# Kernel optimization log

Measured on AMD Instinct MI355X. Metric: run time of the kernel, lower is better.

The kernel has to match this reference:

```python
import jax, jax.numpy as jnp
import numpy as np

B, S, D = 2, 2048, 4096
H, KV, HD = 32, 8, 128          # n_heads, n_kv_heads, head_dim
N_REP = H // KV                  # GQA repeat factor = 4
ROPE_THETA = 500000.0


def _rope_tables(seqlen, head_dim, theta):
    inv_freq = 1.0 / (theta ** (np.arange(0, head_dim, 2, dtype=np.float32) / head_dim))
    angles = np.outer(np.arange(seqlen, dtype=np.float32), inv_freq)  # [S, HD/2]
    return jnp.asarray(np.cos(angles)), jnp.asarray(np.sin(angles))


def setup_inputs() -> dict:
    key = jax.random.key(0)
    ks = jax.random.split(key, 6)
    x = jax.random.normal(ks[0], (B, S, D), dtype=jnp.float32)
    freqs_cos, freqs_sin = _rope_tables(S, HD, ROPE_THETA)
    # causal additive mask, broadcast over (batch, heads)
    mask = jnp.where(jnp.tril(jnp.ones((S, S), dtype=bool)), 0.0, -jnp.inf).astype(jnp.float32)
    sc = 0.02
    wq = sc * jax.random.normal(ks[1], (D, H * HD), dtype=jnp.float32)   # (in, out)
    wk = sc * jax.random.normal(ks[2], (D, KV * HD), dtype=jnp.float32)
    wv = sc * jax.random.normal(ks[3], (D, KV * HD), dtype=jnp.float32)
    wo = sc * jax.random.normal(ks[4], (H * HD, D), dtype=jnp.float32)
    return {"x": x, "freqs_cos": freqs_cos, "freqs_sin": freqs_sin, "mask": mask,
            "wq": wq, "wk": wk, "wv": wv, "wo": wo}


def _apply_rope(t, cos, sin):
    # t: [B, S, nh, HD]; cos/sin: [S, HD/2]. Complex rotation on adjacent pairs.
    t2 = t.reshape(*t.shape[:-1], HD // 2, 2)
    t0, t1 = t2[..., 0], t2[..., 1]
    c = cos[None, :, None, :]
    s = sin[None, :, None, :]
    r0 = t0 * c - t1 * s
    r1 = t0 * s + t1 * c
    return jnp.stack([r0, r1], axis=-1).reshape(t.shape)


def reference(x, freqs_cos, freqs_sin, mask, wq, wk, wv, wo):
    bsz, seqlen, _ = x.shape
    xq = (x @ wq).reshape(bsz, seqlen, H, HD)
    xk = (x @ wk).reshape(bsz, seqlen, KV, HD)
    xv = (x @ wv).reshape(bsz, seqlen, KV, HD)
    xq = _apply_rope(xq, freqs_cos, freqs_sin)
    xk = _apply_rope(xk, freqs_cos, freqs_sin)
    # repeat_kv (GQA) -> [B, S, H, HD]
    keys = jnp.repeat(xk, N_REP, axis=2)
    values = jnp.repeat(xv, N_REP, axis=2)
    scores = jnp.einsum('bqhd,bkhd->bhqk', xq, keys) / jnp.sqrt(jnp.float32(HD))
    scores = scores + mask[None, None, :, :]
    probs = jax.nn.softmax(scores.astype(jnp.float32), axis=-1).astype(xq.dtype)
    out = jnp.einsum('bhqk,bkhd->bqhd', probs, values).reshape(bsz, seqlen, H * HD)
    return out @ wo
```

## Files before the change

### kernel.cpp

```cpp
#include <hip/hip_runtime.h>
#include <stdint.h>

#define B_ 2
#define S_ 2048
#define D_ 4096
#define H_ 32
#define KV_ 8
#define HD_ 128
#define M_ (B_*S_)
#define NQ_ (H_*HD_)
#define NKV_ (KV_*HD_)

typedef unsigned short u16;
typedef __bf16 bf16x8 __attribute__((ext_vector_type(8)));
typedef float f32x4 __attribute__((ext_vector_type(4)));
typedef u16 u16x8 __attribute__((ext_vector_type(8)));
typedef u16 u16x4 __attribute__((ext_vector_type(4)));

__device__ __forceinline__ u16 f2bf(float f) {
  union { float f; unsigned u; } v; v.f = f;
  unsigned r = v.u + 0x7fffu + ((v.u >> 16) & 1u);
  return (u16)(r >> 16);
}
__device__ __forceinline__ u16 f2bft(float f) {
  union { float f; unsigned u; } v; v.f = f;
  return (u16)(v.u >> 16);
}
__device__ __forceinline__ float bf2f(u16 u) {
  union { unsigned u; float f; } v; v.u = ((unsigned)u) << 16;
  return v.f;
}
__device__ __forceinline__ f32x4 mfma16(bf16x8 a, bf16x8 b, f32x4 c) {
  return __builtin_amdgcn_mfma_f32_16x16x32_bf16(a, b, c, 0, 0, 0);
}

#define GLDS16(gp, lp) __builtin_amdgcn_global_load_lds( \
    (const __attribute__((address_space(1))) unsigned int*)(gp), \
    (__attribute__((address_space(3))) unsigned int*)(lp), 16, 0, 0)

__global__ __launch_bounds__(256) void cvt_bf16(const float* __restrict__ in,
                                                u16* __restrict__ out, int n) {
  int i = (blockIdx.x * 256 + threadIdx.x) * 8;
  if (i >= n) return;
  float4 a = *(const float4*)(in + i);
  float4 b = *(const float4*)(in + i + 4);
  u16x8 o;
  o[0]=f2bf(a.x); o[1]=f2bf(a.y); o[2]=f2bf(a.z); o[3]=f2bf(a.w);
  o[4]=f2bf(b.x); o[5]=f2bf(b.y); o[6]=f2bf(b.z); o[7]=f2bf(b.w);
  *(u16x8*)(out + i) = o;
}

__global__ __launch_bounds__(256) void tcvt(const float* __restrict__ in,
                                            u16* __restrict__ out, int R, int C) {
  __shared__ float tf[64][65];
  int c0 = blockIdx.x * 64, r0 = blockIdx.y * 64;
  int l16 = threadIdx.x & 15, r16 = threadIdx.x >> 4;
  #pragma unroll
  for (int p = 0; p < 4; ++p) {
    int r = p * 16 + r16;
    float4 v = *(const float4*)(in + (size_t)(r0 + r) * C + c0 + l16 * 4);
    tf[r][l16 * 4 + 0] = v.x; tf[r][l16 * 4 + 1] = v.y;
    tf[r][l16 * 4 + 2] = v.z; tf[r][l16 * 4 + 3] = v.w;
  }
  __syncthreads();
  int oc = threadIdx.x >> 2, ch = threadIdx.x & 3;
  u16x8 o1, o2;
  #pragma unroll
  for (int i = 0; i < 8; ++i) o1[i] = f2bf(tf[ch * 16 + i][oc]);
  #pragma unroll
  for (int i = 0; i < 8; ++i) o2[i] = f2bf(tf[ch * 16 + 8 + i][oc]);
  *(u16x8*)(out + (size_t)(c0 + oc) * R + r0 + ch * 16) = o1;
  *(u16x8*)(out + (size_t)(c0 + oc) * R + r0 + ch * 16 + 8) = o2;
}

template<int OUTMODE, bool DOROPE>
__global__ __launch_bounds__(512, 2) void gemm256(const u16* __restrict__ A,
    const u16* __restrict__ BT, void* __restrict__ Cv,
    const float* __restrict__ FC, const float* __restrict__ FS,
    int M, int N, int K) {
  extern __shared__ __attribute__((aligned(16))) u16 DL[];
  const int tid = threadIdx.x;
  const int nbx = N >> 8;
  const int cpx = gridDim.x >> 3;
  const int swzb = (blockIdx.x & 7) * cpx + (blockIdx.x >> 3);
  const int bn0 = (swzb % nbx) << 8, bm0 = (swzb / nbx) << 8;
  const int l = tid & 63, g = l >> 4, q = l & 15;
  const int w = tid >> 6;
  const int wm = (w >> 2) * 128, wn = (w & 3) * 64;
  const int nt = K >> 5;
  f32x4 acc[8][4] = {};

  const int srow = tid >> 2, schunk = tid & 3;
  const int ssw = (schunk ^ ((srow >> 1) & 3)) << 3;
  const u16* gA0 = A  + (size_t)(bm0 + srow) * K + ssw;
  const u16* gA1 = gA0 + (size_t)128 * K;
  const u16* gB0 = BT + (size_t)(bn0 + srow) * K + ssw;
  const u16* gB1 = gB0 + (size_t)128 * K;

  auto STAGE = [&](int t) {
    const int kt = t << 5;
    u16* d = DL + (t % 3) * 16384;
    GLDS16(gA0 + kt, d + tid * 8);
    GLDS16(gA1 + kt, d + 4096 + tid * 8);
    GLDS16(gB0 + kt, d + 8192 + tid * 8);
    GLDS16(gB1 + kt, d + 12288 + tid * 8);
  };

  const u16* ra = DL + (wm + q) * 32 + ((g ^ (((wm + q) >> 1) & 3)) << 3);
  const u16* rb = DL + 8192 + (wn + q) * 32 + ((g ^ (((wn + q) >> 1) & 3)) << 3);

  bf16x8 aC[8], aN[8], bC[4], bN[4];

  STAGE(0); STAGE(1);
  asm volatile("s_waitcnt vmcnt(4)" ::: "memory");
  __builtin_amdgcn_s_barrier();
  #pragma unroll
  for (int m = 0; m < 8; ++m) aC[m] = *(const bf16x8*)(ra + m * 512);
  #pragma unroll
  for (int n = 0; n < 4; ++n) bC[n] = *(const bf16x8*)(rb + n * 512);

  auto TILE = [&](int t, bf16x8 (&ac)[8], bf16x8 (&bc)[4],
                         bf16x8 (&an)[8], bf16x8 (&bn)[4]) {
    if (t + 2 < nt) {
      STAGE(t + 2);
      asm volatile("s_waitcnt vmcnt(4)" ::: "memory");
    } else {
      asm volatile("s_waitcnt vmcnt(0)" ::: "memory");
    }
    __builtin_amdgcn_s_barrier();
    if (t + 1 < nt) {
      const u16* pa = ra + ((t + 1) % 3) * 16384;
      const u16* pb = rb + ((t + 1) % 3) * 16384;
      #pragma unroll
      for (int m = 0; m < 8; ++m) an[m] = *(const bf16x8*)(pa + m * 512);
      #pragma unroll
      for (int n = 0; n < 4; ++n) bn[n] = *(const bf16x8*)(pb + n * 512);
    }
    __builtin_amdgcn_s_setprio(1);
    #pragma unroll
    for (int m = 0; m < 8; ++m) {
      acc[m][0] = mfma16(ac[m], bc[0], acc[m][0]);
      acc[m][1] = mfma16(ac[m], bc[1], acc[m][1]);
      acc[m][2] = mfma16(ac[m], bc[2], acc[m][2]);
      acc[m][3] = mfma16(ac[m], bc[3], acc[m][3]);
    }
    __builtin_amdgcn_s_setprio(0);
  };

  for (int t = 0; t < nt; t += 2) {
    TILE(t,     aC, bC, aN, bN);
    TILE(t + 1, aN, bN, aC, bC);
  }

  #pragma unroll
  for (int m = 0; m < 8; ++m)
    #pragma unroll
    for (int n = 0; n < 4; ++n) {
      const int col = bn0 + wn + n * 16 + q;
      if (DOROPE) {
        const int fi = (col & 127) >> 1;
        const float sgn = (q & 1) ? 1.0f : -1.0f;
        #pragma unroll
        for (int j = 0; j < 4; ++j) {
          int row = bm0 + wm + m * 16 + g * 4 + j;
          int pos = row & (S_ - 1);
          float c = FC[pos * 64 + fi], s = FS[pos * 64 + fi];
          float own = acc[m][n][j];
          float par = __shfl_xor(own, 1);
          ((u16*)Cv)[(size_t)row * N + col] = f2bf(own * c + par * s * sgn);
        }
      } else {
        #pragma unroll
        for (int j = 0; j < 4; ++j) {
          size_t off = (size_t)(bm0 + wm + m * 16 + g * 4 + j) * N + col;
          if (OUTMODE == 1) ((float*)Cv)[off] = acc[m][n][j];
          else              ((u16*)Cv)[off]  = f2bf(acc[m][n][j]);
        }
      }
    }
}

__global__ __launch_bounds__(512, 2) void gemm_kv(const u16* __restrict__ A,
    const u16* __restrict__ BT, u16* __restrict__ Ck, u16* __restrict__ Cvt,
    const float* __restrict__ FC, const float* __restrict__ FS,
    int M, int N, int K) {
  extern __shared__ __attribute__((aligned(16))) u16 DL[];
  const int tid = threadIdx.x;
  const int nbx = N >> 7;
  const int cpx = gridDim.x >> 3;
  const int swzb = (blockIdx.x & 7) * cpx + (blockIdx.x >> 3);
  const int bn0 = (swzb % nbx) << 7, bm0 = (swzb / nbx) << 8;
  const int l = tid & 63, g = l >> 4, q = l & 15;
  const int w = tid >> 6;
  const int wm = (w >> 2) * 128, wn = (w & 3) * 32;
  const int nt = K >> 5;
  f32x4 acc[8][2] = {};

  const int srow = tid >> 2, schunk = tid & 3;
  const int ssw = (schunk ^ ((srow >> 1) & 3)) << 3;
  const u16* gA0 = A  + (size_t)(bm0 + srow) * K + ssw;
  const u16* gA1 = gA0 + (size_t)128 * K;
  const u16* gB0 = BT + (size_t)(bn0 + srow) * K + ssw;

  auto STAGE = [&](int t) {
    const int kt = t << 5;
    u16* d = DL + (t % 3) * 12288;
    GLDS16(gA0 + kt, d + tid * 8);
    GLDS16(gA1 + kt, d + 4096 + tid * 8);
    GLDS16(gB0 + kt, d + 8192 + tid * 8);
  };

  const u16* ra = DL + (wm + q) * 32 + ((g ^ (((wm + q) >> 1) & 3)) << 3);
  const u16* rb = DL + 8192 + (wn + q) * 32 + ((g ^ (((wn + q) >> 1) & 3)) << 3);

  bf16x8 aC[8], aN[8], bC[2], bN[2];

  STAGE(0); STAGE(1);
  asm volatile("s_waitcnt vmcnt(3)" ::: "memory");
  __builtin_amdgcn_s_barrier();
  #pragma unroll
  for (int m = 0; m < 8; ++m) aC[m] = *(const bf16x8*)(ra + m * 512);
  #pragma unroll
  for (int n = 0; n < 2; ++n) bC[n] = *(const bf16x8*)(rb + n * 512);

  auto TILE = [&](int t, bf16x8 (&ac)[8], bf16x8 (&bc)[2],
                         bf16x8 (&an)[8], bf16x8 (&bn)[2]) {
    if (t + 2 < nt) {
      STAGE(t + 2);
      asm volatile("s_waitcnt vmcnt(3)" ::: "memory");
    } else {
      asm volatile("s_waitcnt vmcnt(0)" ::: "memory");
    }
    __builtin_amdgcn_s_barrier();
    if (t + 1 < nt) {
      const u16* pa = ra + ((t + 1) % 3) * 12288;
      const u16* pb = rb + ((t + 1) % 3) * 12288;
      #pragma unroll
      for (int m = 0; m < 8; ++m) an[m] = *(const bf16x8*)(pa + m * 512);
      #pragma unroll
      for (int n = 0; n < 2; ++n) bn[n] = *(const bf16x8*)(pb + n * 512);
    }
    __builtin_amdgcn_s_setprio(1);
    #pragma unroll
    for (int m = 0; m < 8; ++m) {
      acc[m][0] = mfma16(ac[m], bc[0], acc[m][0]);
      acc[m][1] = mfma16(ac[m], bc[1], acc[m][1]);
    }
    __builtin_amdgcn_s_setprio(0);
  };

  for (int t = 0; t < nt; t += 2) {
    TILE(t,     aC, bC, aN, bN);
    TILE(t + 1, aN, bN, aC, bC);
  }

  #pragma unroll
  for (int m = 0; m < 8; ++m)
    #pragma unroll
    for (int n = 0; n < 2; ++n) {
      int row0 = bm0 + wm + m * 16 + g * 4;
      int col  = bn0 + wn + n * 16 + q;
      if (col < 1024) {
        const int fi = (col & 127) >> 1;
        const float sgn = (q & 1) ? 1.0f : -1.0f;
        #pragma unroll
        for (int j = 0; j < 4; ++j) {
          int row = row0 + j;
          int pos = row & (S_ - 1);
          float c = FC[pos * 64 + fi], s = FS[pos * 64 + fi];
          float own = acc[m][n][j];
          float par = __shfl_xor(own, 1);
          Ck[(size_t)row * 1024 + col] = f2bf(own * c + par * s * sgn);
        }
      } else {
        int c2 = col - 1024;
        u16x4 pk;
        #pragma unroll
        for (int j = 0; j < 4; ++j) pk[j] = f2bf(acc[m][n][j]);
        size_t off = ((size_t)((row0 >> 11) * KV_ + (c2 >> 7)) * 32 + ((row0 >> 6) & 31)) * 8192
                   + (size_t)(c2 & 127) * 64 + (row0 & 63);
        *(u16x4*)(Cvt + off) = pk;
      }
    }
}

__global__ __launch_bounds__(256, 4) void attn_kernel(
    const u16* __restrict__ Qb, const u16* __restrict__ Kb,
    const u16* __restrict__ VTg, u16* __restrict__ Ob) {
  __shared__ __attribute__((aligned(16))) u16 SM[20480];
  u16* Ks = SM;
  u16* Vs = SM + 8192;
  u16* Ps = SM + 16384;
  const int pr = blockIdx.x;
  const int h = blockIdx.y, b = blockIdx.z;
  const int kvh = h >> 2;
  const int tid = threadIdx.x, w = tid >> 6, l = tid & 63, g = l >> 4, ql = l & 15;
  const float SL2E = 0.08838834764831845f * 1.4426950408889634f;
  const u16* Qh = Qb + (size_t)b * S_ * NQ_ + h * HD_;
  const u16* Kh = Kb + ((size_t)b * S_ * KV_ + kvh) * HD_;
  const u16* Vh = VTg + (size_t)(b * KV_ + kvh) * (32 * 8192);
  u16* Oh = Ob + (size_t)b * S_ * NQ_ + h * HD_;

  for (int ph = 0; ph < 2; ++ph) {
    const int qt = ph ? pr : 31 - pr;
    __syncthreads();
    bf16x8 aq[4];
    #pragma unroll
    for (int kk = 0; kk < 4; ++kk)
      aq[kk] = *(const bf16x8*)(Qh + (size_t)(qt * 64 + w * 16 + ql) * NQ_ + kk * 32 + g * 8);

    f32x4 o[8] = {};
    float mrow = -3.0e38f, lrow = 0.f;

    const int nkt = qt + 1;
    for (int kt = 0; kt < nkt; ++kt) {
      #pragma unroll
      for (int p = 0; p < 4; ++p) {
        int c = tid + p * 256;
        int row = c >> 4, slot = c & 15;
        GLDS16(Kh + (size_t)(kt * 64 + row) * (KV_ * HD_) + ((slot ^ (row & 7)) << 3), Ks + c * 8);
      }
      #pragma unroll
      for (int p = 0; p < 4; ++p) {
        int c = tid + p * 256;
        int row = c >> 3, slot = c & 7;
        GLDS16(Vh + (size_t)kt * 8192 + row * 64 + ((slot ^ (row & 7)) << 3), Vs + c * 8);
      }
      asm volatile("s_waitcnt vmcnt(0)" ::: "memory");
      __builtin_amdgcn_s_barrier();

      if (kt * 64 <= qt * 64 + w * 16 + 15) {
        f32x4 sc[4] = {};
        #pragma unroll
        for (int kk = 0; kk < 4; ++kk) {
          bf16x8 bk[4];
          #pragma unroll
          for (int n = 0; n < 4; ++n) {
            int row = n * 16 + ql;
            bk[n] = *(const bf16x8*)(Ks + row * 128 + (((kk * 4 + g) ^ (row & 7)) << 3));
          }
          #pragma unroll
          for (int n = 0; n < 4; ++n)
            sc[n] = mfma16(bk[n], aq[kk], sc[n]);
        }
        const int qglob = qt * 64 + w * 16 + ql;
        if (kt * 64 + 63 > qt * 64 + w * 16) {
          #pragma unroll
          for (int n = 0; n < 4; ++n)
            #pragma unroll
            for (int j = 0; j < 4; ++j)
              if (kt * 64 + n * 16 + g * 4 + j > qglob) sc[n][j] = -3.0e38f;
        }
        float mx = sc[0][0];
        #pragma unroll
        for (int n = 0; n < 4; ++n)
          #pragma unroll
          for (int j = 0; j < 4; ++j) mx = fmaxf(mx, sc[n][j]);
        mx = fmaxf(mx, __shfl_xor(mx, 16));
        mx = fmaxf(mx, __shfl_xor(mx, 32));
        if (!__all(mx - mrow <= 16.0f)) {
          float mnew = fmaxf(mrow, mx);
          float f = exp2f((mrow - mnew) * SL2E);
          lrow *= f;
          #pragma unroll
          for (int m = 0; m < 8; ++m) o[m] *= f;
          mrow = mnew;
        }
        float rs = 0.f;
        #pragma unroll
        for (int n = 0; n < 4; ++n)
          #pragma unroll
          for (int j = 0; j < 4; ++j) {
            float pv = exp2f((sc[n][j] - mrow) * SL2E);
            sc[n][j] = pv; rs += pv;
          }
        rs += __shfl_xor(rs, 16);
        rs += __shfl_xor(rs, 32);
        lrow += rs;
        u16* Pw = Ps + w * 1024;
        #pragma unroll
        for (int n = 0; n < 4; ++n) {
          u16x4 pk;
          #pragma unroll
          for (int j = 0; j < 4; ++j) pk[j] = f2bft(sc[n][j]);
          *(u16x4*)(Pw + ql * 64 + (((n * 2 + (g >> 1)) ^ (ql & 7)) << 3) + (g & 1) * 4) = pk;
        }
        #pragma unroll
        for (int kk2 = 0; kk2 < 2; ++kk2) {
          bf16x8 bp = *(const bf16x8*)(Pw + ql * 64 + (((kk2 * 4 + g) ^ (ql & 7)) << 3));
          #pragma unroll
          for (int m = 0; m < 8; ++m) {
            int row = m * 16 + ql;
            bf16x8 av = *(const bf16x8*)(Vs + row * 64 + (((kk2 * 4 + g) ^ (row & 7)) << 3));
            o[m] = mfma16(av, bp, o[m]);
          }
        }
      }
      __builtin_amdgcn_s_barrier();
    }
    __syncthreads();
    u16* OS = SM;
    float linv = 1.0f / lrow;
    #pragma unroll
    for (int m = 0; m < 8; ++m)
      #pragma unroll
      for (int j = 0; j < 4; ++j)
        OS[(w * 16 + ql) * 136 + m * 16 + g * 4 + j] = f2bf(o[m][j] * linv);
    __syncthreads();
    #pragma unroll
    for (int p = 0; p < 4; ++p) {
      int c = tid + p * 256;
      int row = c >> 4, col8 = c & 15;
      u16x8 d = *(const u16x8*)(OS + row * 136 + col8 * 8);
      *(u16x8*)(Oh + (size_t)(qt * 64 + row) * NQ_ + col8 * 8) = d;
    }
  }
}

extern "C" void kernel_launch(void* const* d_in, const int* in_sizes, int n_in,
                              void* d_out, int out_size, void* d_ws, size_t ws_size,
                              hipStream_t stream) {
  const float* x  = (const float*)d_in[0];
  const float* fc = (const float*)d_in[1];
  const float* fs = (const float*)d_in[2];
  const float* wq = (const float*)d_in[4];
  const float* wk = (const float*)d_in[5];
  const float* wv = (const float*)d_in[6];
  const float* wo = (const float*)d_in[7];

  char* ws = (char*)d_ws;
  u16* xb  = (u16*)(ws + 0);
  u16* wqT = (u16*)(ws + 33554432);
  u16* wkT = (u16*)(ws + 67108864);
  u16* wvT = (u16*)(ws + 75497472);
  u16* woT = (u16*)(ws + 83886080);
  u16* qb  = (u16*)(ws + 117440512);
  u16* kb  = (u16*)(ws + 150994944);
  u16* vtg = (u16*)(ws + 159383552);
  u16* ob  = (u16*)(ws + 167772160);
  if (ws_size < 201326592u) return;

  cvt_bf16<<<(M_ * D_) / (8 * 256), 256, 0, stream>>>(x, xb, M_ * D_);
  tcvt<<<dim3(NQ_ / 64, D_ / 64), 256, 0, stream>>>(wq, wqT, D_, NQ_);
  tcvt<<<dim3(NKV_ / 64, D_ / 64), 256, 0, stream>>>(wk, wkT, D_, NKV_);
  tcvt<<<dim3(NKV_ / 64, D_ / 64), 256, 0, stream>>>(wv, wvT, D_, NKV_);
  tcvt<<<dim3(D_ / 64, NQ_ / 64), 256, 0, stream>>>(wo, woT, NQ_, D_);

  gemm256<0, true><<<(NQ_ / 256) * (M_ / 256), 512, 98304, stream>>>(
      xb, wqT, qb, fc, fs, M_, NQ_, D_);
  gemm_kv<<<(2048 / 128) * (M_ / 256), 512, 73728, stream>>>(
      xb, wkT, kb, vtg, fc, fs, M_, 2048, D_);

  attn_kernel<<<dim3(16, H_, B_), 256, 0, stream>>>(qb, kb, vtg, ob);

  gemm256<1, false><<<(D_ / 256) * (M_ / 256), 512, 98304, stream>>>(
      ob, woT, d_out, fc, fs, M_, D_, NQ_);
}
```

Baseline: 514.9 us.

## Restructure gemm256 to BK=64 double-buffered pipeline with interleaved sub-stage loads

The 256x256 GEMM mainloop now uses a K tile of 64 instead of 32, with two LDS buffers of 64 KB each instead of three 32 KB buffers, and an 8-chunk XOR swizzle. Each K tile is split into four phases of 2x4x2 MFMAs. Global-to-LDS loads for A (next tile) and B (tile after next) are spread across those phases, with barriers in between, instead of being issued once per tile. The goal is fewer loop iterations and barriers per unit of K and better overlap of loads with MFMA work. The trade-off is 128 KB of dynamic LDS, which may block the two-blocks-per-CU occupancy the launch bounds ask for, plus more barriers inside each tile.

```diff
diff --git a/kernel.cpp b/kernel.cpp
--- a/kernel.cpp
+++ b/kernel.cpp
@@ -87,69 +87,90 @@
   const int l = tid & 63, g = l >> 4, q = l & 15;
   const int w = tid >> 6;
   const int wm = (w >> 2) * 128, wn = (w & 3) * 64;
-  const int nt = K >> 5;
+  const int nt = K >> 6;
   f32x4 acc[8][4] = {};
 
-  const int srow = tid >> 2, schunk = tid & 3;
-  const int ssw = (schunk ^ ((srow >> 1) & 3)) << 3;
-  const u16* gA0 = A  + (size_t)(bm0 + srow) * K + ssw;
-  const u16* gA1 = gA0 + (size_t)128 * K;
-  const u16* gB0 = BT + (size_t)(bn0 + srow) * K + ssw;
-  const u16* gB1 = gB0 + (size_t)128 * K;
-
-  auto STAGE = [&](int t) {
-    const int kt = t << 5;
-    u16* d = DL + (t % 3) * 16384;
-    GLDS16(gA0 + kt, d + tid * 8);
-    GLDS16(gA1 + kt, d + 4096 + tid * 8);
-    GLDS16(gB0 + kt, d + 8192 + tid * 8);
-    GLDS16(gB1 + kt, d + 12288 + tid * 8);
+  const int srow = tid >> 3, slot = tid & 7;
+  const int ssw = (slot ^ (srow & 7)) << 3;
+  const u16* gA = A  + (size_t)(bm0 + srow) * K + ssw;
+  const u16* gB = BT + (size_t)(bn0 + srow) * K + ssw;
+
+  auto STG = [&](const u16* gbase, int oB, int h, int t) {
+    const int kt = t << 6;
+    u16* d = DL + (t & 1) * 32768 + oB * 16384 + h * 8192 + tid * 8;
+    GLDS16(gbase + (size_t)(h * 128) * K + kt, d);
+    GLDS16(gbase + (size_t)(h * 128 + 64) * K + kt, d + 4096);
   };
 
-  const u16* ra = DL + (wm + q) * 32 + ((g ^ (((wm + q) >> 1) & 3)) << 3);
-  const u16* rb = DL + 8192 + (wn + q) * 32 + ((g ^ (((wn + q) >> 1) & 3)) << 3);
-
-  bf16x8 aC[8], aN[8], bC[4], bN[4];
-
-  STAGE(0); STAGE(1);
+  const u16* ra0 = DL + (wm + q) * 64 + ((g ^ (q & 7)) << 3);
+  const u16* ra1 = DL + (wm + q) * 64 + (((4 + g) ^ (q & 7)) << 3);
+  const u16* rb0 = DL + 16384 + (wn + q) * 64 + ((g ^ (q & 7)) << 3);
+  const u16* rb1 = DL + 16384 + (wn + q) * 64 + (((4 + g) ^ (q & 7)) << 3);
+
+  STG(gA, 0, 0, 0); STG(gA, 0, 1, 0);
+  STG(gB, 1, 0, 0); STG(gB, 1, 1, 0);
+  STG(gB, 1, 0, 1); STG(gB, 1, 1, 1);
   asm volatile("s_waitcnt vmcnt(4)" ::: "memory");
   __builtin_amdgcn_s_barrier();
-  #pragma unroll
-  for (int m = 0; m < 8; ++m) aC[m] = *(const bf16x8*)(ra + m * 512);
-  #pragma unroll
-  for (int n = 0; n < 4; ++n) bC[n] = *(const bf16x8*)(rb + n * 512);
-
-  auto TILE = [&](int t, bf16x8 (&ac)[8], bf16x8 (&bc)[4],
-                         bf16x8 (&an)[8], bf16x8 (&bn)[4]) {
-    if (t + 2 < nt) {
-      STAGE(t + 2);
-      asm volatile("s_waitcnt vmcnt(4)" ::: "memory");
-    } else {
-      asm volatile("s_waitcnt vmcnt(0)" ::: "memory");
-    }
+
+  for (int t = 0; t < nt; ++t) {
+    const int bo = (t & 1) * 32768;
+    bf16x8 bf[4][2], ap[2][2];
+    #pragma unroll
+    for (int n = 0; n < 4; ++n) {
+      bf[n][0] = *(const bf16x8*)(rb0 + bo + n * 1024);
+      bf[n][1] = *(const bf16x8*)(rb1 + bo + n * 1024);
+    }
+    ap[0][0] = *(const bf16x8*)(ra0 + bo);
+    ap[0][1] = *(const bf16x8*)(ra1 + bo);
+    ap[1][0] = *(const bf16x8*)(ra0 + bo + 1024);
+    ap[1][1] = *(const bf16x8*)(ra1 + bo + 1024);
+    if (t + 1 < nt) STG(gA, 0, 0, t + 1);
     __builtin_amdgcn_s_barrier();
+    asm volatile("s_waitcnt lgkmcnt(0)" ::: "memory");
+    __builtin_amdgcn_sched_barrier(0);
+    __builtin_amdgcn_s_setprio(1);
+    #pragma unroll
+    for (int mm = 0; mm < 2; ++mm)
+      #pragma unroll
+      for (int n = 0; n < 4; ++n) {
+        acc[mm][n] = mfma16(ap[mm][0], bf[n][0], acc[mm][n]);
+        acc[mm][n] = mfma16(ap[mm][1], bf[n][1], acc[mm][n]);
+      }
+    __builtin_amdgcn_s_setprio(0);
+    __builtin_amdgcn_s_barrier();
+    #pragma unroll
+    for (int p = 1; p < 4; ++p) {
+      const int mb = 2 * p;
+      ap[0][0] = *(const bf16x8*)(ra0 + bo + mb * 1024);
+      ap[0][1] = *(const bf16x8*)(ra1 + bo + mb * 1024);
+      ap[1][0] = *(const bf16x8*)(ra0 + bo + (mb + 1) * 1024);
+      ap[1][1] = *(const bf16x8*)(ra1 + bo + (mb + 1) * 1024);
+      if (p == 1 && t + 1 < nt) STG(gA, 0, 1, t + 1);
+      if (p == 2 && t + 2 < nt) STG(gB, 1, 0, t + 2);
+      if (p == 3 && t + 2 < nt) STG(gB, 1, 1, t + 2);
+      __builtin_amdgcn_s_barrier();
+      asm volatile("s_waitcnt lgkmcnt(0)" ::: "memory");
+      __builtin_amdgcn_sched_barrier(0);
+      __builtin_amdgcn_s_setprio(1);
+      #pragma unroll
+      for (int mm = 0; mm < 2; ++mm)
+        #pragma unroll
+        for (int n = 0; n < 4; ++n) {
+          acc[mb + mm][n] = mfma16(ap[mm][0], bf[n][0], acc[mb + mm][n]);
+          acc[mb + mm][n] = mfma16(ap[mm][1], bf[n][1], acc[mb + mm][n]);
+        }
+      __builtin_amdgcn_s_setprio(0);
+      if (p < 3) __builtin_amdgcn_s_barrier();
+    }
     if (t + 1 < nt) {
-      const u16* pa = ra + ((t + 1) % 3) * 16384;
-      const u16* pb = rb + ((t + 1) % 3) * 16384;
-      #pragma unroll
-      for (int m = 0; m < 8; ++m) an[m] = *(const bf16x8*)(pa + m * 512);
-      #pragma unroll
-      for (int n = 0; n < 4; ++n) bn[n] = *(const bf16x8*)(pb + n * 512);
-    }
-    __builtin_amdgcn_s_setprio(1);
-    #pragma unroll
-    for (int m = 0; m < 8; ++m) {
-      acc[m][0] = mfma16(ac[m], bc[0], acc[m][0]);
-      acc[m][1] = mfma16(ac[m], bc[1], acc[m][1]);
-      acc[m][2] = mfma16(ac[m], bc[2], acc[m][2]);
-      acc[m][3] = mfma16(ac[m], bc[3], acc[m][3]);
-    }
-    __builtin_amdgcn_s_setprio(0);
-  };
-
-  for (int t = 0; t < nt; t += 2) {
-    TILE(t,     aC, bC, aN, bN);
-    TILE(t + 1, aN, bN, aC, bC);
+      if (t + 2 < nt) {
+        asm volatile("s_waitcnt vmcnt(4)" ::: "memory");
+      } else {
+        asm volatile("s_waitcnt vmcnt(0)" ::: "memory");
+      }
+      __builtin_amdgcn_s_barrier();
+    }
   }
 
   #pragma unroll
@@ -446,13 +467,13 @@
   tcvt<<<dim3(NKV_ / 64, D_ / 64), 256, 0, stream>>>(wv, wvT, D_, NKV_);
   tcvt<<<dim3(D_ / 64, NQ_ / 64), 256, 0, stream>>>(wo, woT, NQ_, D_);
 
-  gemm256<0, true><<<(NQ_ / 256) * (M_ / 256), 512, 98304, stream>>>(
+  gemm256<0, true><<<(NQ_ / 256) * (M_ / 256), 512, 131072, stream>>>(
       xb, wqT, qb, fc, fs, M_, NQ_, D_);
   gemm_kv<<<(2048 / 128) * (M_ / 256), 512, 73728, stream>>>(
       xb, wkT, kb, vtg, fc, fs, M_, 2048, D_);
 
   attn_kernel<<<dim3(16, H_, B_), 256, 0, stream>>>(qb, kb, vtg, ob);
 
-  gemm256<1, false><<<(D_ / 256) * (M_ / 256), 512, 98304, stream>>>(
+  gemm256<1, false><<<(D_ / 256) * (M_ / 256), 512, 131072, stream>>>(
       ob, woT, d_out, fc, fs, M_, D_, NQ_);
 }
```

Result: no change. 508.7 us (-1.2%).
